# Optimization experiments

Hardware: AMD Instinct MI355X
Metric: run time of the kernel (lower is better)

Reference implementation:

```python
import jax, jax.numpy as jnp
import numpy as np

WS = 14            # window height/width
CLS = 1            # cls tokens
DIM = 768
H = 12             # heads
DH = DIM // H      # head dim = 64
B = 128
N = WS * WS + CLS  # 197
SCALE = DH ** (-0.5)
TABLE = (2 * WS - 1) ** 2 + CLS  # 730


def _rel_index():
    # Swin-style relative position index, with CLS rows/cols pointing at the
    # last table entry (torch uses index -1 which wraps to TABLE-1).
    c = np.arange(WS)
    coords = np.stack(np.meshgrid(c, c, indexing='ij'))      # [2,14,14]
    cf = coords.reshape(2, -1)                                # [2,196]
    rel = cf[:, :, None] - cf[:, None, :]                     # [2,196,196]
    rel = rel.transpose(1, 2, 0).astype(np.int64)             # [196,196,2]
    rel[..., 0] += WS - 1
    rel[..., 1] += WS - 1
    rel[..., 0] *= 2 * WS - 1
    idx = rel.sum(-1)                                         # [196,196]
    full = np.full((N, N), -1, np.int64)
    full[CLS:, CLS:] = idx
    full = np.where(full < 0, TABLE - 1, full)
    return jnp.asarray(full, jnp.int32)


def setup_inputs() -> dict:
    key = jax.random.key(0)
    ks = jax.random.split(key, 5)
    return {
        'x': jax.random.normal(ks[0], (B, N, DIM), jnp.float32),
        'qkv_w': jax.random.normal(ks[1], (3 * DIM, DIM), jnp.float32) * 0.02,
        'proj_w': jax.random.normal(ks[2], (DIM, DIM), jnp.float32) * 0.02,
        'proj_b': jnp.zeros((DIM,), jnp.float32),
        'bias_table': jax.random.normal(ks[3], (TABLE, H), jnp.float32) * 0.02,
        'rel_idx': _rel_index(),
    }


def reference(x, qkv_w, proj_w, proj_b, bias_table, rel_idx):
    Bc, Nc, C = x.shape
    qkv = x @ qkv_w.T                                   # [B,N,3C]
    qkv = qkv.reshape(Bc, Nc, 3, H, DH).transpose(2, 0, 3, 1, 4)
    q, k, v = qkv[0], qkv[1], qkv[2]                    # [B,H,N,D]
    attn = jnp.einsum('bhnd,bhmd->bhnm', q, k) * SCALE  # [B,H,N,N]
    bias = bias_table[rel_idx]                          # [N,N,H]
    attn = attn + bias.transpose(2, 0, 1)[None]         # broadcast over batch
    attn = jax.nn.softmax(attn, axis=-1)
    out = jnp.einsum('bhnm,bhmd->bhnd', attn, v)        # [B,H,N,D]
    out = out.transpose(0, 2, 1, 3).reshape(Bc, Nc, C)
    return out @ proj_w.T + proj_b
```

## Files before the change

### kernel.cpp

```cpp
#include <hip/hip_runtime.h>
#include <hip/hip_bf16.h>

typedef _Float16 half8 __attribute__((ext_vector_type(8)));
typedef _Float16 half4 __attribute__((ext_vector_type(4)));
typedef float floatx4 __attribute__((ext_vector_type(4)));

#define MFMA16(a, b, c) __builtin_amdgcn_mfma_f32_16x16x32_f16(a, b, c, 0, 0, 0)
#define GLDS16(gp, lp) __builtin_amdgcn_global_load_lds( \
    (const __attribute__((address_space(1))) void*)(gp), \
    (__attribute__((address_space(3))) void*)(lp), 16, 0, 0)

#define BATCH 128
#define NTOK 197
#define DIM 768
#define NH 12
#define DH 64
#define TABLE 730
#define M_ROWS (BATCH * NTOK)
#define KPAD 224
#define NKT 13

__global__ void cvt_f32_f16(const float* __restrict__ src, _Float16* __restrict__ dst, int n4) {
    int i = blockIdx.x * 256 + threadIdx.x;
    if (i < n4) {
        float4 v = ((const float4*)src)[i];
        half4 o;
        o[0] = (_Float16)v.x; o[1] = (_Float16)v.y;
        o[2] = (_Float16)v.z; o[3] = (_Float16)v.w;
        ((half4*)dst)[i] = o;
    }
}

__global__ void bias_pre(const float* __restrict__ table, const int* __restrict__ ridx,
                         float* __restrict__ biasp) {
    int idx = blockIdx.x * 256 + threadIdx.x;
    if (idx >= NH * NTOK * KPAD) return;
    int h = idx / (NTOK * KPAD);
    int rem = idx - h * (NTOK * KPAD);
    int i = rem / KPAD;
    int j = rem - i * KPAD;
    float v = -1.0e30f;
    if (j < NTOK) v = table[ridx[i * NTOK + j] * NH + h];
    biasp[idx] = v;
}

__device__ __forceinline__ void gemm_core_768(const _Float16* __restrict__ A,
                                              const _Float16* __restrict__ B,
                                              int m0b, int n0b,
                                              _Float16* As, _Float16* Bs,
                                              floatx4 acc[4][4]) {
    const int lane = threadIdx.x & 63;
    const int w = threadIdx.x >> 6;
    const int r = lane & 15, q = lane >> 4;
    const int mo = (w & 1) * 64;
    const int no = (w >> 1) * 64;
    const int srow = w * 32 + (lane >> 3);
    const int gatom = (lane & 7) ^ (lane >> 3);
    const int rx = r & 7;

    const _Float16* pa[4];
    const _Float16* pb[4];
#pragma unroll
    for (int c = 0; c < 4; ++c) {
        pa[c] = A + (size_t)(m0b + srow + c * 8) * DIM + gatom * 8;
        pb[c] = B + (size_t)(n0b + srow + c * 8) * DIM + gatom * 8;
    }
    _Float16* ldsA = As + w * 2048;
    _Float16* ldsB = Bs + w * 2048;

    for (int kk = 0; kk < DIM / 64; ++kk) {
#pragma unroll
        for (int c = 0; c < 4; ++c) {
            GLDS16(pa[c], ldsA + c * 512);
            GLDS16(pb[c], ldsB + c * 512);
            pa[c] += 64;
            pb[c] += 64;
        }
        __syncthreads();
#pragma unroll
        for (int s = 0; s < 2; ++s) {
            half8 a[4], b[4];
#pragma unroll
            for (int i = 0; i < 4; ++i)
                a[i] = *(const half8*)&As[((mo + i * 16 + r) * 8 + ((s * 4 + q) ^ rx)) * 8];
#pragma unroll
            for (int j = 0; j < 4; ++j)
                b[j] = *(const half8*)&Bs[((no + j * 16 + r) * 8 + ((s * 4 + q) ^ rx)) * 8];
#pragma unroll
            for (int i = 0; i < 4; ++i)
#pragma unroll
                for (int j = 0; j < 4; ++j)
                    acc[i][j] = MFMA16(a[i], b[j], acc[i][j]);
        }
        __syncthreads();
    }
}

__global__ __launch_bounds__(256) void qkv_gemm(const _Float16* __restrict__ X,
                                                const _Float16* __restrict__ W,
                                                _Float16* __restrict__ qh,
                                                _Float16* __restrict__ kh,
                                                _Float16* __restrict__ vh) {
    __shared__ __align__(16) _Float16 As[128 * 64];
    __shared__ __align__(16) _Float16 Bs[128 * 64];
    const int lane = threadIdx.x & 63;
    const int w = threadIdx.x >> 6;
    const int r = lane & 15, q = lane >> 4;

    floatx4 acc[4][4] = {};
    gemm_core_768(X, W, blockIdx.y * 128, blockIdx.x * 128, As, Bs, acc);

    const int m0 = blockIdx.y * 128 + (w & 1) * 64;
    const int n0 = blockIdx.x * 128 + (w >> 1) * 64;
    const int which = n0 / 768;
    const int hh = (n0 % 768) / 64;
    _Float16* dst = (which == 0) ? qh : ((which == 1) ? kh : vh);
    const float scale = (which == 0) ? 0.125f : 1.0f;
#pragma unroll
    for (int i = 0; i < 4; ++i) {
#pragma unroll
        for (int rr = 0; rr < 4; ++rr) {
            int grow = m0 + i * 16 + q * 4 + rr;
            int b_idx = grow / 197;
            int n_idx = grow - b_idx * 197;
            size_t rowoff = ((size_t)(b_idx * NH + hh) * NTOK + n_idx) * DH;
#pragma unroll
            for (int j = 0; j < 4; ++j) {
                int d0 = j * 16 + r;
                dst[rowoff + d0] = (_Float16)(acc[i][j][rr] * scale);
            }
        }
    }
}

__global__ __launch_bounds__(256) void proj_gemm(const _Float16* __restrict__ A,
                                                 const _Float16* __restrict__ W,
                                                 const float* __restrict__ bias,
                                                 float* __restrict__ out) {
    __shared__ __align__(16) _Float16 As[128 * 64];
    __shared__ __align__(16) _Float16 Bs[128 * 64];
    const int lane = threadIdx.x & 63;
    const int w = threadIdx.x >> 6;
    const int r = lane & 15, q = lane >> 4;

    floatx4 acc[4][4] = {};
    gemm_core_768(A, W, blockIdx.y * 128, blockIdx.x * 128, As, Bs, acc);

    const int m0 = blockIdx.y * 128 + (w & 1) * 64;
    const int n0 = blockIdx.x * 128 + (w >> 1) * 64;
#pragma unroll
    for (int i = 0; i < 4; ++i) {
#pragma unroll
        for (int rr = 0; rr < 4; ++rr) {
            size_t grow = m0 + i * 16 + q * 4 + rr;
#pragma unroll
            for (int j = 0; j < 4; ++j) {
                int gcol = n0 + j * 16 + r;
                out[grow * DIM + gcol] = acc[i][j][rr] + bias[gcol];
            }
        }
    }
}

__global__ __launch_bounds__(256) void attn_kernel(const _Float16* __restrict__ qh,
                                                   const _Float16* __restrict__ kh,
                                                   const _Float16* __restrict__ vh,
                                                   const float* __restrict__ biasp,
                                                   _Float16* __restrict__ ah) {
    __shared__ __align__(16) _Float16 Vt[64][232];
    __shared__ __align__(16) _Float16 P[4][16][232];

    const int bh = blockIdx.x;
    const int b = bh / NH, h = bh - b * NH;
    const int tid = threadIdx.x;
    const int w = tid >> 6, lane = tid & 63;
    const int r = lane & 15, q = lane >> 4;
    const size_t base = (size_t)bh * NTOK * DH;
    const _Float16* Qb = qh + base;
    const _Float16* Kb = kh + base;
    const _Float16* Vb = vh + base;

    for (int idx = tid; idx < KPAD * DH; idx += 256) {
        int j = idx >> 6, d = idx & 63;
        Vt[d][j] = (j < NTOK) ? Vb[(size_t)j * DH + d] : (_Float16)0.0f;
    }
    __syncthreads();

    for (int it = 0; it < 4; ++it) {
        int qt = it * 4 + w;
        bool active = qt < NKT;
        floatx4 oacc[4] = {};
        if (active) {
            half8 aq0 = {}, aq1 = {};
            int rowq = qt * 16 + r;
            if (rowq < NTOK) {
                aq0 = *(const half8*)(Qb + (size_t)rowq * DH + q * 8);
                aq1 = *(const half8*)(Qb + (size_t)rowq * DH + 32 + q * 8);
            }
            floatx4 sacc[NKT] = {};
#pragma unroll
            for (int nt = 0; nt < NKT; ++nt) {
                half8 b0 = {}, b1 = {};
                int rowk = nt * 16 + r;
                if (rowk < NTOK) {
                    b0 = *(const half8*)(Kb + (size_t)rowk * DH + q * 8);
                    b1 = *(const half8*)(Kb + (size_t)rowk * DH + 32 + q * 8);
                }
                sacc[nt] = MFMA16(aq0, b0, sacc[nt]);
                sacc[nt] = MFMA16(aq1, b1, sacc[nt]);
            }
#pragma unroll
            for (int rr = 0; rr < 4; ++rr) {
                int irow = qt * 16 + q * 4 + rr;
                if (irow > NTOK - 1) irow = NTOK - 1;
                const float* bp = biasp + ((size_t)h * NTOK + irow) * KPAD + r;
                float sv[NKT];
                float mx = -3.0e38f;
#pragma unroll
                for (int nt = 0; nt < NKT; ++nt) {
                    float s = sacc[nt][rr] + bp[nt * 16];
                    sv[nt] = s;
                    mx = fmaxf(mx, s);
                }
#pragma unroll
                for (int msk = 1; msk <= 8; msk <<= 1) mx = fmaxf(mx, __shfl_xor(mx, msk, 64));
                float sum = 0.f;
#pragma unroll
                for (int nt = 0; nt < NKT; ++nt) {
                    float e = __expf(sv[nt] - mx);
                    sv[nt] = e;
                    sum += e;
                }
#pragma unroll
                for (int msk = 1; msk <= 8; msk <<= 1) sum += __shfl_xor(sum, msk, 64);
                float inv = 1.0f / sum;
                int prow = q * 4 + rr;
#pragma unroll
                for (int nt = 0; nt < NKT; ++nt)
                    P[w][prow][nt * 16 + r] = (_Float16)(sv[nt] * inv);
                P[w][prow][208 + r] = (_Float16)0.0f;
            }
        }
        __syncthreads();
        if (active) {
#pragma unroll
            for (int kt = 0; kt < 7; ++kt) {
                half8 ap = *(const half8*)&P[w][r][kt * 32 + q * 8];
#pragma unroll
                for (int dt = 0; dt < 4; ++dt) {
                    half8 bv = *(const half8*)&Vt[dt * 16 + r][kt * 32 + q * 8];
                    oacc[dt] = MFMA16(ap, bv, oacc[dt]);
                }
            }
#pragma unroll
            for (int rr = 0; rr < 4; ++rr) {
                int rowq = qt * 16 + q * 4 + rr;
                if (rowq < NTOK) {
                    size_t o = ((size_t)b * NTOK + rowq) * DIM + h * DH;
#pragma unroll
                    for (int dt = 0; dt < 4; ++dt)
                        ah[o + dt * 16 + r] = (_Float16)oacc[dt][rr];
                }
            }
        }
        __syncthreads();
    }
}

extern "C" void kernel_launch(void* const* d_in, const int* in_sizes, int n_in,
                              void* d_out, int out_size, void* d_ws, size_t ws_size,
                              hipStream_t stream) {
    const float* x = (const float*)d_in[0];
    const float* qkv_w = (const float*)d_in[1];
    const float* proj_w = (const float*)d_in[2];
    const float* proj_b = (const float*)d_in[3];
    const float* table = (const float*)d_in[4];
    const int* ridx = (const int*)d_in[5];
    float* out = (float*)d_out;

    char* ws = (char*)d_ws;
    const size_t SZ_X = (size_t)M_ROWS * DIM * 2;
    const size_t SZ_WQKV = (size_t)3 * DIM * DIM * 2;
    const size_t SZ_WPROJ = (size_t)DIM * DIM * 2;
    const size_t SZ_HEAD = (size_t)BATCH * NH * NTOK * DH * 2;
    const size_t SZ_BIAS = (size_t)NH * NTOK * KPAD * 4;

    _Float16* xh = (_Float16*)(ws + 0);
    _Float16* ah = (_Float16*)(ws + 0);
    _Float16* wqkvh = (_Float16*)(ws + SZ_X);
    _Float16* wprojh = (_Float16*)(ws + SZ_X + SZ_WQKV);
    _Float16* qh = (_Float16*)(ws + SZ_X + SZ_WQKV + SZ_WPROJ);
    _Float16* kh = (_Float16*)(ws + SZ_X + SZ_WQKV + SZ_WPROJ + SZ_HEAD);
    _Float16* vh = (_Float16*)(ws + SZ_X + SZ_WQKV + SZ_WPROJ + 2 * SZ_HEAD);
    float* biasp = (float*)(ws + SZ_X + SZ_WQKV + SZ_WPROJ + 3 * SZ_HEAD);
    (void)SZ_BIAS; (void)ws_size; (void)n_in; (void)in_sizes; (void)out_size;

    {
        int n4 = M_ROWS * DIM / 4;
        cvt_f32_f16<<<(n4 + 255) / 256, 256, 0, stream>>>(x, xh, n4);
        n4 = 3 * DIM * DIM / 4;
        cvt_f32_f16<<<(n4 + 255) / 256, 256, 0, stream>>>(qkv_w, wqkvh, n4);
        n4 = DIM * DIM / 4;
        cvt_f32_f16<<<(n4 + 255) / 256, 256, 0, stream>>>(proj_w, wprojh, n4);
    }
    {
        int n = NH * NTOK * KPAD;
        bias_pre<<<(n + 255) / 256, 256, 0, stream>>>(table, ridx, biasp);
    }
    {
        dim3 grid(3 * DIM / 128, M_ROWS / 128);
        qkv_gemm<<<grid, 256, 0, stream>>>(xh, wqkvh, qh, kh, vh);
    }
    attn_kernel<<<BATCH * NH, 256, 0, stream>>>(qh, kh, vh, biasp, ah);
    {
        dim3 grid(DIM / 128, M_ROWS / 128);
        proj_gemm<<<grid, 256, 0, stream>>>(ah, wprojh, proj_b, out);
    }
}
```

Before: 460.0 us.

## Store V transposed, pre-swizzle fp16 bias, and split attention per wave tile

The QKV GEMM now writes V directly in a transposed [bh][d][KPAD] layout, so the attention kernel no longer transposes V through LDS. The relative bias is precomputed as fp16 in MFMA fragment order, so each lane fetches it with one half4 load per key tile. Each wave now handles one independent 16-row query tile, giving many more, smaller blocks without block-wide barriers; P only goes through a small per-wave LDS buffer. The transposed V store is strided and uncoalesced, which may slow the GEMM epilogue. The padded V columns are never zeroed and rely on P being zero there.

After: 468.6 us. Within noise of the previous version (+1.9%).

```diff
diff --git a/kernel.cpp b/kernel.cpp
--- a/kernel.cpp
+++ b/kernel.cpp
@@ -15,10 +15,10 @@
 #define DIM 768
 #define NH 12
 #define DH 64
-#define TABLE 730
 #define M_ROWS (BATCH * NTOK)
 #define KPAD 224
 #define NKT 13
+#define NTILES (BATCH * NH * NKT)
 
 __global__ void cvt_f32_f16(const float* __restrict__ src, _Float16* __restrict__ dst, int n4) {
     int i = blockIdx.x * 256 + threadIdx.x;
@@ -32,16 +32,21 @@
 }
 
 __global__ void bias_pre(const float* __restrict__ table, const int* __restrict__ ridx,
-                         float* __restrict__ biasp) {
+                         _Float16* __restrict__ biasph) {
     int idx = blockIdx.x * 256 + threadIdx.x;
-    if (idx >= NH * NTOK * KPAD) return;
-    int h = idx / (NTOK * KPAD);
-    int rem = idx - h * (NTOK * KPAD);
-    int i = rem / KPAD;
-    int j = rem - i * KPAD;
-    float v = -1.0e30f;
-    if (j < NTOK) v = table[ridx[i * NTOK + j] * NH + h];
-    biasp[idx] = v;
+    if (idx >= NH * 13 * 13 * 256) return;
+    int e = idx & 255;
+    int r = e >> 4, q = (e >> 2) & 3, rr = e & 3;
+    int t = idx >> 8;
+    int nt = t % 13; int t2 = t / 13; int qt = t2 % 13; int h = t2 / 13;
+    int row = qt * 16 + q * 4 + rr;
+    int col = nt * 16 + r;
+    float v = -30000.0f;
+    if (col < NTOK) {
+        int rc = row < NTOK ? row : NTOK - 1;
+        v = table[ridx[rc * NTOK + col] * NH + h];
+    }
+    biasph[idx] = (_Float16)v;
 }
 
 __device__ __forceinline__ void gemm_core_768(const _Float16* __restrict__ A,
@@ -100,7 +105,7 @@
                                                 const _Float16* __restrict__ W,
                                                 _Float16* __restrict__ qh,
                                                 _Float16* __restrict__ kh,
-                                                _Float16* __restrict__ vh) {
+                                                _Float16* __restrict__ vt) {
     __shared__ __align__(16) _Float16 As[128 * 64];
     __shared__ __align__(16) _Float16 Bs[128 * 64];
     const int lane = threadIdx.x & 63;
@@ -114,20 +119,34 @@
     const int n0 = blockIdx.x * 128 + (w >> 1) * 64;
     const int which = n0 / 768;
     const int hh = (n0 % 768) / 64;
-    _Float16* dst = (which == 0) ? qh : ((which == 1) ? kh : vh);
-    const float scale = (which == 0) ? 0.125f : 1.0f;
-#pragma unroll
-    for (int i = 0; i < 4; ++i) {
-#pragma unroll
-        for (int rr = 0; rr < 4; ++rr) {
-            int grow = m0 + i * 16 + q * 4 + rr;
-            int b_idx = grow / 197;
-            int n_idx = grow - b_idx * 197;
-            size_t rowoff = ((size_t)(b_idx * NH + hh) * NTOK + n_idx) * DH;
-#pragma unroll
-            for (int j = 0; j < 4; ++j) {
-                int d0 = j * 16 + r;
-                dst[rowoff + d0] = (_Float16)(acc[i][j][rr] * scale);
+    if (which < 2) {
+        _Float16* dst = (which == 0) ? qh : kh;
+        const float scale = (which == 0) ? 0.125f : 1.0f;
+#pragma unroll
+        for (int i = 0; i < 4; ++i) {
+#pragma unroll
+            for (int rr = 0; rr < 4; ++rr) {
+                int grow = m0 + i * 16 + q * 4 + rr;
+                int b_idx = grow / 197;
+                int n_idx = grow - b_idx * 197;
+                size_t rowoff = ((size_t)(b_idx * NH + hh) * NTOK + n_idx) * DH;
+#pragma unroll
+                for (int j = 0; j < 4; ++j)
+                    dst[rowoff + j * 16 + r] = (_Float16)(acc[i][j][rr] * scale);
+            }
+        }
+    } else {
+#pragma unroll
+        for (int i = 0; i < 4; ++i) {
+#pragma unroll
+            for (int rr = 0; rr < 4; ++rr) {
+                int grow = m0 + i * 16 + q * 4 + rr;
+                int b_idx = grow / 197;
+                int n_idx = grow - b_idx * 197;
+                size_t hbase = (size_t)(b_idx * NH + hh) * DH;
+#pragma unroll
+                for (int j = 0; j < 4; ++j)
+                    vt[(hbase + j * 16 + r) * KPAD + n_idx] = (_Float16)acc[i][j][rr];
             }
         }
     }
@@ -164,106 +183,100 @@
 
 __global__ __launch_bounds__(256) void attn_kernel(const _Float16* __restrict__ qh,
                                                    const _Float16* __restrict__ kh,
-                                                   const _Float16* __restrict__ vh,
-                                                   const float* __restrict__ biasp,
+                                                   const _Float16* __restrict__ vt,
+                                                   const _Float16* __restrict__ biasph,
                                                    _Float16* __restrict__ ah) {
-    __shared__ __align__(16) _Float16 Vt[64][232];
-    __shared__ __align__(16) _Float16 P[4][16][232];
-
-    const int bh = blockIdx.x;
+    __shared__ __align__(16) _Float16 P[4][16][40];
+    const int w = threadIdx.x >> 6, lane = threadIdx.x & 63;
+    const int r = lane & 15, q = lane >> 4;
+    const int T = blockIdx.x * 4 + w;
+    const int bh = T / 13;
+    const int qt = T - bh * 13;
     const int b = bh / NH, h = bh - b * NH;
-    const int tid = threadIdx.x;
-    const int w = tid >> 6, lane = tid & 63;
-    const int r = lane & 15, q = lane >> 4;
-    const size_t base = (size_t)bh * NTOK * DH;
-    const _Float16* Qb = qh + base;
-    const _Float16* Kb = kh + base;
-    const _Float16* Vb = vh + base;
-
-    for (int idx = tid; idx < KPAD * DH; idx += 256) {
-        int j = idx >> 6, d = idx & 63;
-        Vt[d][j] = (j < NTOK) ? Vb[(size_t)j * DH + d] : (_Float16)0.0f;
-    }
-    __syncthreads();
-
-    for (int it = 0; it < 4; ++it) {
-        int qt = it * 4 + w;
-        bool active = qt < NKT;
-        floatx4 oacc[4] = {};
-        if (active) {
-            half8 aq0 = {}, aq1 = {};
-            int rowq = qt * 16 + r;
-            if (rowq < NTOK) {
-                aq0 = *(const half8*)(Qb + (size_t)rowq * DH + q * 8);
-                aq1 = *(const half8*)(Qb + (size_t)rowq * DH + 32 + q * 8);
-            }
-            floatx4 sacc[NKT] = {};
-#pragma unroll
-            for (int nt = 0; nt < NKT; ++nt) {
-                half8 b0 = {}, b1 = {};
-                int rowk = nt * 16 + r;
-                if (rowk < NTOK) {
-                    b0 = *(const half8*)(Kb + (size_t)rowk * DH + q * 8);
-                    b1 = *(const half8*)(Kb + (size_t)rowk * DH + 32 + q * 8);
-                }
-                sacc[nt] = MFMA16(aq0, b0, sacc[nt]);
-                sacc[nt] = MFMA16(aq1, b1, sacc[nt]);
-            }
-#pragma unroll
-            for (int rr = 0; rr < 4; ++rr) {
-                int irow = qt * 16 + q * 4 + rr;
-                if (irow > NTOK - 1) irow = NTOK - 1;
-                const float* bp = biasp + ((size_t)h * NTOK + irow) * KPAD + r;
-                float sv[NKT];
-                float mx = -3.0e38f;
-#pragma unroll
-                for (int nt = 0; nt < NKT; ++nt) {
-                    float s = sacc[nt][rr] + bp[nt * 16];
-                    sv[nt] = s;
-                    mx = fmaxf(mx, s);
-                }
-#pragma unroll
-                for (int msk = 1; msk <= 8; msk <<= 1) mx = fmaxf(mx, __shfl_xor(mx, msk, 64));
-                float sum = 0.f;
-#pragma unroll
-                for (int nt = 0; nt < NKT; ++nt) {
-                    float e = __expf(sv[nt] - mx);
-                    sv[nt] = e;
-                    sum += e;
-                }
-#pragma unroll
-                for (int msk = 1; msk <= 8; msk <<= 1) sum += __shfl_xor(sum, msk, 64);
-                float inv = 1.0f / sum;
-                int prow = q * 4 + rr;
-#pragma unroll
-                for (int nt = 0; nt < NKT; ++nt)
-                    P[w][prow][nt * 16 + r] = (_Float16)(sv[nt] * inv);
-                P[w][prow][208 + r] = (_Float16)0.0f;
-            }
-        }
-        __syncthreads();
-        if (active) {
-#pragma unroll
-            for (int kt = 0; kt < 7; ++kt) {
-                half8 ap = *(const half8*)&P[w][r][kt * 32 + q * 8];
-#pragma unroll
-                for (int dt = 0; dt < 4; ++dt) {
-                    half8 bv = *(const half8*)&Vt[dt * 16 + r][kt * 32 + q * 8];
-                    oacc[dt] = MFMA16(ap, bv, oacc[dt]);
-                }
-            }
-#pragma unroll
-            for (int rr = 0; rr < 4; ++rr) {
-                int rowq = qt * 16 + q * 4 + rr;
-                if (rowq < NTOK) {
-                    size_t o = ((size_t)b * NTOK + rowq) * DIM + h * DH;
-#pragma unroll
-                    for (int dt = 0; dt < 4; ++dt)
-                        ah[o + dt * 16 + r] = (_Float16)oacc[dt][rr];
-                }
-            }
-        }
-        __syncthreads();
+    const _Float16* Qb = qh + (size_t)bh * NTOK * DH;
+    const _Float16* Kb = kh + (size_t)bh * NTOK * DH;
+    const _Float16* Vtb = vt + (size_t)bh * DH * KPAD;
+
+    half4 bf[NKT];
+    const _Float16* bbase = biasph + (((size_t)h * 13 + qt) * 13) * 256 + r * 16 + q * 4;
+#pragma unroll
+    for (int nt = 0; nt < NKT; ++nt)
+        bf[nt] = *(const half4*)(bbase + nt * 256);
+
+    const int rowq = qt * 16 + r;
+    half8 aq0 = *(const half8*)(Qb + (size_t)rowq * DH + q * 8);
+    half8 aq1 = *(const half8*)(Qb + (size_t)rowq * DH + 32 + q * 8);
+
+    floatx4 sacc[NKT] = {};
+#pragma unroll
+    for (int nt = 0; nt < NKT; ++nt) {
+        half8 b0 = {}, b1 = {};
+        int rowk = nt * 16 + r;
+        if (rowk < NTOK) {
+            b0 = *(const half8*)(Kb + (size_t)rowk * DH + q * 8);
+            b1 = *(const half8*)(Kb + (size_t)rowk * DH + 32 + q * 8);
+        }
+        sacc[nt] = MFMA16(aq0, b0, sacc[nt]);
+        sacc[nt] = MFMA16(aq1, b1, sacc[nt]);
+    }
+
+    _Float16 pv[NKT][4];
+#pragma unroll
+    for (int rr = 0; rr < 4; ++rr) {
+        float sv[NKT];
+        float mx = -3.0e38f;
+#pragma unroll
+        for (int nt = 0; nt < NKT; ++nt) {
+            float s = sacc[nt][rr] + (float)bf[nt][rr];
+            sv[nt] = s;
+            mx = fmaxf(mx, s);
+        }
+#pragma unroll
+        for (int m = 1; m <= 8; m <<= 1) mx = fmaxf(mx, __shfl_xor(mx, m, 64));
+        float sm = 0.f;
+#pragma unroll
+        for (int nt = 0; nt < NKT; ++nt) {
+            float e = __expf(sv[nt] - mx);
+            sv[nt] = e;
+            sm += e;
+        }
+#pragma unroll
+        for (int m = 1; m <= 8; m <<= 1) sm += __shfl_xor(sm, m, 64);
+        float inv = 1.0f / sm;
+#pragma unroll
+        for (int nt = 0; nt < NKT; ++nt)
+            pv[nt][rr] = (_Float16)(sv[nt] * inv);
+    }
+
+    floatx4 oacc[4] = {};
+    _Float16* Pw = &P[w][0][0];
+#pragma unroll
+    for (int kt = 0; kt < 7; ++kt) {
+        const int nt0 = kt * 2, nt1 = kt * 2 + 1;
+#pragma unroll
+        for (int rr = 0; rr < 4; ++rr) {
+            Pw[(q * 4 + rr) * 40 + r] = pv[nt0][rr];
+            Pw[(q * 4 + rr) * 40 + 16 + r] = (nt1 < NKT) ? pv[nt1][rr] : (_Float16)0.0f;
+        }
+        __asm__ volatile("" ::: "memory");
+        half8 ap = *(const half8*)&Pw[r * 40 + q * 8];
+        __asm__ volatile("" ::: "memory");
+#pragma unroll
+        for (int dt = 0; dt < 4; ++dt) {
+            half8 bv = *(const half8*)(Vtb + (size_t)(dt * 16 + r) * KPAD + kt * 32 + q * 8);
+            oacc[dt] = MFMA16(ap, bv, oacc[dt]);
+        }
+    }
+
+#pragma unroll
+    for (int rr = 0; rr < 4; ++rr) {
+        int row = qt * 16 + q * 4 + rr;
+        if (row < NTOK) {
+            size_t o = ((size_t)b * NTOK + row) * DIM + h * DH;
+#pragma unroll
+            for (int dt = 0; dt < 4; ++dt)
+                ah[o + dt * 16 + r] = (_Float16)oacc[dt][rr];
+        }
     }
 }
 
@@ -283,7 +296,8 @@
     const size_t SZ_WQKV = (size_t)3 * DIM * DIM * 2;
     const size_t SZ_WPROJ = (size_t)DIM * DIM * 2;
     const size_t SZ_HEAD = (size_t)BATCH * NH * NTOK * DH * 2;
-    const size_t SZ_BIAS = (size_t)NH * NTOK * KPAD * 4;
+    const size_t SZ_VT = (size_t)BATCH * NH * DH * KPAD * 2;
+    const size_t SZ_BIAS = (size_t)NH * 13 * 13 * 256 * 2;
 
     _Float16* xh = (_Float16*)(ws + 0);
     _Float16* ah = (_Float16*)(ws + 0);
@@ -291,8 +305,8 @@
     _Float16* wprojh = (_Float16*)(ws + SZ_X + SZ_WQKV);
     _Float16* qh = (_Float16*)(ws + SZ_X + SZ_WQKV + SZ_WPROJ);
     _Float16* kh = (_Float16*)(ws + SZ_X + SZ_WQKV + SZ_WPROJ + SZ_HEAD);
-    _Float16* vh = (_Float16*)(ws + SZ_X + SZ_WQKV + SZ_WPROJ + 2 * SZ_HEAD);
-    float* biasp = (float*)(ws + SZ_X + SZ_WQKV + SZ_WPROJ + 3 * SZ_HEAD);
+    _Float16* vt = (_Float16*)(ws + SZ_X + SZ_WQKV + SZ_WPROJ + 2 * SZ_HEAD);
+    _Float16* biasph = (_Float16*)(ws + SZ_X + SZ_WQKV + SZ_WPROJ + 2 * SZ_HEAD + SZ_VT);
     (void)SZ_BIAS; (void)ws_size; (void)n_in; (void)in_sizes; (void)out_size;
 
     {
@@ -304,14 +318,14 @@
         cvt_f32_f16<<<(n4 + 255) / 256, 256, 0, stream>>>(proj_w, wprojh, n4);
     }
     {
-        int n = NH * NTOK * KPAD;
-        bias_pre<<<(n + 255) / 256, 256, 0, stream>>>(table, ridx, biasp);
+        int n = NH * 13 * 13 * 256;
+        bias_pre<<<(n + 255) / 256, 256, 0, stream>>>(table, ridx, biasph);
     }
     {
         dim3 grid(3 * DIM / 128, M_ROWS / 128);
-        qkv_gemm<<<grid, 256, 0, stream>>>(xh, wqkvh, qh, kh, vh);
-    }
-    attn_kernel<<<BATCH * NH, 256, 0, stream>>>(qh, kh, vh, biasp, ah);
+        qkv_gemm<<<grid, 256, 0, stream>>>(xh, wqkvh, qh, kh, vt);
+    }
+    attn_kernel<<<NTILES / 4, 256, 0, stream>>>(qh, kh, vt, biasph, ah);
     {
         dim3 grid(DIM / 128, M_ROWS / 128);
         proj_gemm<<<grid, 256, 0, stream>>>(ah, wprojh, proj_b, out);
```
